# Kernel optimization log

Hardware: AMD Instinct MI355X
Metric: run time of the kernel (lower is better)

## Reference

```python
import jax, jax.numpy as jnp
import numpy as np

C_FINE, C_MID, C_COARSE = 100, 20, 5
EPS = 1e-12


def setup_inputs() -> dict:
    key = jax.random.key(0)
    k1, k2 = jax.random.split(key)
    N, D = 262144, 128
    representations = jax.random.normal(k1, (N, D), dtype=jnp.float32)
    target_fine = jax.random.randint(k2, (N,), 0, C_FINE, dtype=jnp.int32)
    # nested hierarchy: fine -> mid (5 fines per mid), fine -> coarse (20 fines per coarse)
    fine2mid = (jnp.arange(C_FINE, dtype=jnp.int32) // (C_FINE // C_MID)).astype(jnp.int32)
    fine2coarse = (jnp.arange(C_FINE, dtype=jnp.int32) // (C_FINE // C_COARSE)).astype(jnp.int32)
    return {
        "representations": representations,
        "target_fine": target_fine,
        "fine2mid": fine2mid,
        "fine2coarse": fine2coarse,
    }


def _safe_norm(diff):
    # L2 norm along last axis; eps gives a 0 subgradient at diff==0
    return jnp.sqrt(jnp.sum(diff * diff, axis=-1) + EPS)


def _segment_mean(x, ids, num_segments):
    ones = jnp.ones(x.shape[:1], x.dtype)
    s = jax.ops.segment_sum(x, ids, num_segments=num_segments)
    c = jax.ops.segment_sum(ones, ids, num_segments=num_segments)
    return s / jnp.maximum(c, 1.0)[:, None]


def reference(representations, target_fine, fine2mid, fine2coarse):
    # ---- tree construction (vectorized version of the per-class Python loops) ----
    # fine prototypes: mean of representations per fine class  [C_FINE, D]
    fine_protos = _segment_mean(representations, target_fine, C_FINE)
    # mid prototypes: mean of child fine prototypes  [C_MID, D]
    mid_protos = _segment_mean(fine_protos, fine2mid, C_MID)
    # coarse prototypes: mean of child mid prototypes  [C_COARSE, D]
    mid2coarse = jax.ops.segment_max(fine2coarse, fine2mid, num_segments=C_MID)
    coarse_protos = _segment_mean(mid_protos, mid2coarse, C_COARSE)
    # (the root node contributes ||root - root|| = 0 to every pair, so it is omitted)

    # ---- pairwise tree-path distances over all fine-class pairs ----
    iu, ju = np.triu_indices(C_FINE, k=1)  # static C*(C-1)/2 = 4950 pairs
    ci, cj = fine2coarse[iu], fine2coarse[ju]
    mi, mj = fine2mid[iu], fine2mid[ju]
    tree_d = _safe_norm(coarse_protos[ci] - coarse_protos[cj]) \
           + _safe_norm(mid_protos[mi] - mid_protos[mj])
    # Euclidean distances between fine prototypes
    proto_d = _safe_norm(fine_protos[iu] - fine_protos[ju])

    # ---- CPCC: loss = 1 - Pearson correlation(tree_d, proto_d) ----
    tc = tree_d - jnp.mean(tree_d)
    pc = proto_d - jnp.mean(proto_d)
    corr = jnp.sum(tc * pc) / jnp.sqrt(jnp.sum(tc * tc) * jnp.sum(pc * pc) + EPS)
    return 1.0 - corr
```

## Files before the change

kernel.cpp:

```cpp
#include <hip/hip_runtime.h>
#include <math.h>

#define C_FINE   100
#define C_MID    20
#define C_COARSE 5
#define D        128
#define NROWS    262144
#define NPAIRS   4950
#define NBLK4    78

#define NB       512
#define ROWS_PB  (NROWS/NB)
#define NSTEP    (ROWS_PB/32)
#define MT       7
#define PSTR2    (113*128)

#define FP_OFF    0
#define DM_OFF    12800
#define DC_OFF    13200
#define ACC_OFF   13232
#define DONE_OFF  13244
#define CNT_OFF   13248
#define FSUM_OFF  13376
#define PART_OFF  26176

typedef __attribute__((ext_vector_type(8))) short bf16x8;
typedef __attribute__((ext_vector_type(4))) float f32x4;

static __device__ __forceinline__ unsigned short f2bf(float f) {
    unsigned int x = __float_as_uint(f);
    x += 0x7FFF + ((x >> 16) & 1);
    return (unsigned short)(x >> 16);
}

__global__ __launch_bounds__(256) void kMF(const float* __restrict__ rep,
                                           const int* __restrict__ tgt,
                                           float* __restrict__ ws) {
    __shared__ int hist[128];
    const int t  = threadIdx.x;
    const int w  = t >> 6;
    const int l  = t & 63;
    const int lg = l >> 4;
    const int ll = l & 15;
    const int blk   = blockIdx.x;
    const int rbase = blk * ROWS_PB;

    if (t < 128) hist[t] = 0;
    __syncthreads();
    atomicAdd(&hist[tgt[rbase + t]], 1);
    atomicAdd(&hist[tgt[rbase + t + 256]], 1);

    const int colbase = 32 * w + ll;

    f32x4 acc[MT][2];
    #pragma unroll
    for (int m = 0; m < MT; ++m)
        #pragma unroll
        for (int n = 0; n < 2; ++n)
            #pragma unroll
            for (int i = 0; i < 4; ++i) acc[m][n][i] = 0.f;

    float vA[16], vB[16];
    int   tA[8],  tB[8];

#define LOADSTEP(V, T, s) do {                                                  \
    const float* p_ = rep + ((size_t)(rbase + (s) * 32 + 8 * lg) * D + colbase);\
    _Pragma("unroll")                                                           \
    for (int j_ = 0; j_ < 8; ++j_) {                                            \
        V[j_]     = p_[j_ * D];                                                 \
        V[8 + j_] = p_[j_ * D + 16];                                            \
    }                                                                           \
    const int* q_ = tgt + (rbase + (s) * 32 + 8 * lg);                          \
    _Pragma("unroll")                                                           \
    for (int j_ = 0; j_ < 8; ++j_) T[j_] = q_[j_];                              \
} while (0)

#define COMPSTEP(V, T) do {                                                     \
    bf16x8 b0_, b1_;                                                            \
    _Pragma("unroll")                                                           \
    for (int j_ = 0; j_ < 8; ++j_) {                                            \
        b0_[j_] = (short)f2bf(V[j_]);                                           \
        b1_[j_] = (short)f2bf(V[8 + j_]);                                       \
    }                                                                           \
    _Pragma("unroll")                                                           \
    for (int m_ = 0; m_ < MT; ++m_) {                                           \
        const int cb_ = 16 * m_ + ll;                                           \
        bf16x8 a_;                                                              \
        _Pragma("unroll")                                                       \
        for (int j_ = 0; j_ < 8; ++j_)                                          \
            a_[j_] = (T[j_] == cb_) ? (short)0x3F80 : (short)0;                 \
        acc[m_][0] = __builtin_amdgcn_mfma_f32_16x16x32_bf16(a_, b0_, acc[m_][0], 0, 0, 0); \
        acc[m_][1] = __builtin_amdgcn_mfma_f32_16x16x32_bf16(a_, b1_, acc[m_][1], 0, 0, 0); \
    }                                                                           \
} while (0)

    LOADSTEP(vA, tA, 0);
    #pragma unroll 1
    for (int s = 0; s < NSTEP; s += 2) {
        LOADSTEP(vB, tB, s + 1);
        COMPSTEP(vA, tA);
        if (s + 2 < NSTEP) LOADSTEP(vA, tA, s + 2);
        COMPSTEP(vB, tB);
    }
#undef LOADSTEP
#undef COMPSTEP

    float* part = ws + PART_OFF + (size_t)blk * PSTR2;
    #pragma unroll
    for (int m = 0; m < MT; ++m)
        #pragma unroll
        for (int n = 0; n < 2; ++n)
            #pragma unroll
            for (int i = 0; i < 4; ++i)
                part[(16 * m + 4 * lg + i) * D + 32 * w + 16 * n + ll] = acc[m][n][i];
    __syncthreads();
    if (t < 128) part[112 * D + t] = (t < C_FINE) ? (float)hist[t] : 0.f;
}

__global__ __launch_bounds__(512) void kRed(float* __restrict__ ws) {
    const int c = blockIdx.x;
    const int t = threadIdx.x;
    const int g = t >> 7, d = t & 127;
    float s = 0.f;
    #pragma unroll 8
    for (int b = g; b < NB; b += 4)
        s += ws[PART_OFF + (size_t)b * PSTR2 + c * D + d];
    __shared__ float red[4][128];
    red[g][d] = s;

    float cv = ws[PART_OFF + (size_t)t * PSTR2 + 112 * D + c];
    #pragma unroll
    for (int off = 32; off > 0; off >>= 1) cv += __shfl_down(cv, off);
    __shared__ float cw[8];
    if ((t & 63) == 0) cw[t >> 6] = cv;
    __syncthreads();
    if (g == 0) ws[FSUM_OFF + c * D + d] = red[0][d] + red[1][d] + red[2][d] + red[3][d];
    if (t == 0) {
        float tot = 0.f;
        #pragma unroll
        for (int q = 0; q < 8; ++q) tot += cw[q];
        ws[CNT_OFF + c] = tot;
    }
}

__global__ __launch_bounds__(256) void k3_hier(const int* __restrict__ f2m,
                                               const int* __restrict__ f2c,
                                               float* __restrict__ ws) {
    __shared__ float fineP[C_FINE][D];
    __shared__ float midP[C_MID][D + 1];
    __shared__ float coarP[C_COARSE][D + 1];
    __shared__ int   sf2m[C_FINE], sf2c[C_FINE], m2c[C_MID];
    __shared__ float midCnt[C_MID], coarCnt[C_COARSE];
    __shared__ float sTot[C_FINE];
    const int t = threadIdx.x;

    if (t < C_FINE) {
        sf2m[t] = f2m[t]; sf2c[t] = f2c[t];
        sTot[t] = ws[CNT_OFF + t];
    }
    for (int e = t; e < C_MID * (D + 1); e += 256) ((float*)midP)[e] = 0.f;
    for (int e = t; e < C_COARSE * (D + 1); e += 256) ((float*)coarP)[e] = 0.f;
    __syncthreads();

    for (int e = t; e < C_FINE * D; e += 256) {
        int c = e >> 7, d = e & 127;
        float v = ws[FSUM_OFF + e] / fmaxf(sTot[c], 1.f);
        fineP[c][d] = v;
        ws[FP_OFF + e] = v;
    }
    if (t < C_MID) {
        int cntv = 0, mx = -2147483647;
        for (int f = 0; f < C_FINE; ++f)
            if (sf2m[f] == t) { ++cntv; mx = max(mx, sf2c[f]); }
        midCnt[t] = (float)max(cntv, 1);
        m2c[t] = mx;
    }
    __syncthreads();

    if (t < D) {
        const int d = t;
        for (int f = 0; f < C_FINE; ++f)
            midP[sf2m[f]][d] += fineP[f][d];
        for (int m = 0; m < C_MID; ++m)
            midP[m][d] /= midCnt[m];
    }
    if (t >= 128 && t < 128 + C_COARSE) {
        int cc = t - 128, cntv = 0;
        for (int m = 0; m < C_MID; ++m) if (m2c[m] == cc) ++cntv;
        coarCnt[cc] = (float)max(cntv, 1);
    }
    __syncthreads();

    if (t < D) {
        const int d = t;
        for (int m = 0; m < C_MID; ++m)
            coarP[m2c[m]][d] += midP[m][d];
        for (int cc = 0; cc < C_COARSE; ++cc)
            coarP[cc][d] /= coarCnt[cc];
    }
    __syncthreads();

    for (int e = t; e < C_MID * C_MID; e += 256) {
        int m1 = e / C_MID, m2 = e % C_MID;
        float ss = 0.f;
        #pragma unroll 8
        for (int d = 0; d < D; ++d) {
            float df = midP[m1][d] - midP[m2][d];
            ss += df * df;
        }
        ws[DM_OFF + e] = sqrtf(ss + 1e-12f);
    }
    for (int e = t; e < C_COARSE * C_COARSE; e += 256) {
        int c1 = e / C_COARSE, c2 = e % C_COARSE;
        float ss = 0.f;
        #pragma unroll 8
        for (int d = 0; d < D; ++d) {
            float df = coarP[c1][d] - coarP[c2][d];
            ss += df * df;
        }
        ws[DC_OFF + e] = sqrtf(ss + 1e-12f);
    }
    if (t < 5) ((double*)(ws + ACC_OFF))[t] = 0.0;
    if (t == 5) ((int*)ws + DONE_OFF)[0] = 0;
}

__global__ __launch_bounds__(64) void k45_pairs(float* __restrict__ ws,
                                                const int* __restrict__ f2m,
                                                const int* __restrict__ f2c,
                                                float* __restrict__ out) {
    const int p = blockIdx.x * 64 + threadIdx.x;
    double st = 0, sp = 0, stp = 0, stt = 0, spp = 0;
    if (p < NPAIRS) {
        int i = 0, rem = p;
        while (rem >= C_FINE - 1 - i) { rem -= C_FINE - 1 - i; ++i; }
        int j = i + 1 + rem;

        const float4* Fi = (const float4*)(ws + FP_OFF + i * D);
        const float4* Fj = (const float4*)(ws + FP_OFF + j * D);
        float ss = 0.f;
        #pragma unroll
        for (int k = 0; k < D / 4; ++k) {
            float4 a = Fi[k], b = Fj[k];
            float dx = a.x - b.x, dy = a.y - b.y, dz = a.z - b.z, dw = a.w - b.w;
            ss += dx * dx + dy * dy + dz * dz + dw * dw;
        }
        float proto = sqrtf(ss + 1e-12f);
        float tree  = ws[DC_OFF + f2c[i] * C_COARSE + f2c[j]]
                    + ws[DM_OFF + f2m[i] * C_MID + f2m[j]];
        st = tree; sp = proto;
        stp = (double)tree * (double)proto;
        stt = (double)tree * (double)tree;
        spp = (double)proto * (double)proto;
    }
    for (int off = 32; off > 0; off >>= 1) {
        st  += __shfl_down(st, off);
        sp  += __shfl_down(sp, off);
        stp += __shfl_down(stp, off);
        stt += __shfl_down(stt, off);
        spp += __shfl_down(spp, off);
    }
    if (threadIdx.x == 0) {
        double* acc = (double*)(ws + ACC_OFF);
        atomicAdd(&acc[0], st);
        atomicAdd(&acc[1], sp);
        atomicAdd(&acc[2], stp);
        atomicAdd(&acc[3], stt);
        atomicAdd(&acc[4], spp);
        __threadfence();
        int* done = (int*)ws + DONE_OFF;
        int ticket = atomicAdd(done, 1);
        if (ticket == NBLK4 - 1) {
            double fst  = atomicAdd(&acc[0], 0.0);
            double fsp  = atomicAdd(&acc[1], 0.0);
            double fstp = atomicAdd(&acc[2], 0.0);
            double fstt = atomicAdd(&acc[3], 0.0);
            double fspp = atomicAdd(&acc[4], 0.0);
            const double n = (double)NPAIRS;
            double num = fstp - fst * fsp / n;
            double dtt = fstt - fst * fst / n;
            double dpp = fspp - fsp * fsp / n;
            double corr = num / sqrt(dtt * dpp + 1e-12);
            out[0] = (float)(1.0 - corr);
        }
    }
}

extern "C" void kernel_launch(void* const* d_in, const int* in_sizes, int n_in,
                              void* d_out, int out_size, void* d_ws, size_t ws_size,
                              hipStream_t stream) {
    const float* rep = (const float*)d_in[0];
    const int*   tgt = (const int*)d_in[1];
    const int*   f2m = (const int*)d_in[2];
    const int*   f2c = (const int*)d_in[3];
    float* ws  = (float*)d_ws;
    float* out = (float*)d_out;

    hipLaunchKernelGGL(kMF,       dim3(NB),     dim3(256), 0, stream, rep, tgt, ws);
    hipLaunchKernelGGL(kRed,      dim3(C_FINE), dim3(512), 0, stream, ws);
    hipLaunchKernelGGL(k3_hier,   dim3(1),      dim3(256), 0, stream, f2m, f2c, ws);
    hipLaunchKernelGGL(k45_pairs, dim3(NBLK4),  dim3(64),  0, stream,
                       ws, f2m, f2c, out);
}
```

Before: 81.99 us.

## Stage representation tiles through LDS with coalesced float4 loads in kMF

The segment-sum MFMA kernel now uses 512 threads per block, each wave owning 16 columns instead of 32. Each 32-row tile is loaded with coalesced float4 global reads into a double-buffered LDS tile, and targets are cached in LDS once. Previously each lane issued strided scalar global loads. The change aims to improve global memory coalescing and latency hiding. In exchange it adds LDS traffic and a __syncthreads per step.

Result: slower. 86.38 us (+5.4%).

```diff
diff --git a/kernel.cpp b/kernel.cpp
--- a/kernel.cpp
+++ b/kernel.cpp
@@ -33,10 +33,12 @@
     return (unsigned short)(x >> 16);
 }
 
-__global__ __launch_bounds__(256) void kMF(const float* __restrict__ rep,
-                                           const int* __restrict__ tgt,
-                                           float* __restrict__ ws) {
-    __shared__ int hist[128];
+__global__ __launch_bounds__(512, 4) void kMF(const float* __restrict__ rep,
+                                              const int* __restrict__ tgt,
+                                              float* __restrict__ ws) {
+    __shared__ float tile[2][32 * 128];
+    __shared__ int   ltgt[ROWS_PB];
+    __shared__ int   hist[128];
     const int t  = threadIdx.x;
     const int w  = t >> 6;
     const int l  = t & 63;
@@ -47,73 +49,72 @@
 
     if (t < 128) hist[t] = 0;
     __syncthreads();
-    atomicAdd(&hist[tgt[rbase + t]], 1);
-    atomicAdd(&hist[tgt[rbase + t + 256]], 1);
-
-    const int colbase = 32 * w + ll;
-
-    f32x4 acc[MT][2];
+    {
+        int c = tgt[rbase + t];
+        ltgt[t] = c;
+        atomicAdd(&hist[c], 1);
+    }
+
+    const float4* rep4 = (const float4*)rep;
+    const int tile4base = rbase * (D / 4);
+
+    f32x4 acc[MT];
     #pragma unroll
     for (int m = 0; m < MT; ++m)
         #pragma unroll
-        for (int n = 0; n < 2; ++n)
+        for (int i = 0; i < 4; ++i) acc[m][i] = 0.f;
+
+    {
+        float4 a0 = rep4[tile4base + t];
+        float4 a1 = rep4[tile4base + 512 + t];
+        ((float4*)tile[0])[t]       = a0;
+        ((float4*)tile[0])[t + 512] = a1;
+    }
+    __syncthreads();
+
+    #pragma unroll 1
+    for (int s = 0; s < NSTEP; ++s) {
+        const int buf = s & 1;
+        float4 na, nb;
+        if (s + 1 < NSTEP) {
+            na = rep4[tile4base + (s + 1) * 1024 + t];
+            nb = rep4[tile4base + (s + 1) * 1024 + 512 + t];
+        }
+
+        const float* tf = tile[buf];
+        float vB[8];
+        int   tv[8];
+        #pragma unroll
+        for (int j = 0; j < 8; ++j) {
+            vB[j] = tf[(8 * lg + j) * D + 16 * w + ll];
+            tv[j] = ltgt[s * 32 + 8 * lg + j];
+        }
+        bf16x8 b0;
+        #pragma unroll
+        for (int j = 0; j < 8; ++j) b0[j] = (short)f2bf(vB[j]);
+        #pragma unroll
+        for (int m = 0; m < MT; ++m) {
+            const int cb = 16 * m + ll;
+            bf16x8 a;
             #pragma unroll
-            for (int i = 0; i < 4; ++i) acc[m][n][i] = 0.f;
-
-    float vA[16], vB[16];
-    int   tA[8],  tB[8];
-
-#define LOADSTEP(V, T, s) do {                                                  \
-    const float* p_ = rep + ((size_t)(rbase + (s) * 32 + 8 * lg) * D + colbase);\
-    _Pragma("unroll")                                                           \
-    for (int j_ = 0; j_ < 8; ++j_) {                                            \
-        V[j_]     = p_[j_ * D];                                                 \
-        V[8 + j_] = p_[j_ * D + 16];                                            \
-    }                                                                           \
-    const int* q_ = tgt + (rbase + (s) * 32 + 8 * lg);                          \
-    _Pragma("unroll")                                                           \
-    for (int j_ = 0; j_ < 8; ++j_) T[j_] = q_[j_];                              \
-} while (0)
-
-#define COMPSTEP(V, T) do {                                                     \
-    bf16x8 b0_, b1_;                                                            \
-    _Pragma("unroll")                                                           \
-    for (int j_ = 0; j_ < 8; ++j_) {                                            \
-        b0_[j_] = (short)f2bf(V[j_]);                                           \
-        b1_[j_] = (short)f2bf(V[8 + j_]);                                       \
-    }                                                                           \
-    _Pragma("unroll")                                                           \
-    for (int m_ = 0; m_ < MT; ++m_) {                                           \
-        const int cb_ = 16 * m_ + ll;                                           \
-        bf16x8 a_;                                                              \
-        _Pragma("unroll")                                                       \
-        for (int j_ = 0; j_ < 8; ++j_)                                          \
-            a_[j_] = (T[j_] == cb_) ? (short)0x3F80 : (short)0;                 \
-        acc[m_][0] = __builtin_amdgcn_mfma_f32_16x16x32_bf16(a_, b0_, acc[m_][0], 0, 0, 0); \
-        acc[m_][1] = __builtin_amdgcn_mfma_f32_16x16x32_bf16(a_, b1_, acc[m_][1], 0, 0, 0); \
-    }                                                                           \
-} while (0)
-
-    LOADSTEP(vA, tA, 0);
-    #pragma unroll 1
-    for (int s = 0; s < NSTEP; s += 2) {
-        LOADSTEP(vB, tB, s + 1);
-        COMPSTEP(vA, tA);
-        if (s + 2 < NSTEP) LOADSTEP(vA, tA, s + 2);
-        COMPSTEP(vB, tB);
-    }
-#undef LOADSTEP
-#undef COMPSTEP
+            for (int j = 0; j < 8; ++j)
+                a[j] = (tv[j] == cb) ? (short)0x3F80 : (short)0;
+            acc[m] = __builtin_amdgcn_mfma_f32_16x16x32_bf16(a, b0, acc[m], 0, 0, 0);
+        }
+
+        if (s + 1 < NSTEP) {
+            ((float4*)tile[buf ^ 1])[t]       = na;
+            ((float4*)tile[buf ^ 1])[t + 512] = nb;
+        }
+        __syncthreads();
+    }
 
     float* part = ws + PART_OFF + (size_t)blk * PSTR2;
     #pragma unroll
     for (int m = 0; m < MT; ++m)
         #pragma unroll
-        for (int n = 0; n < 2; ++n)
-            #pragma unroll
-            for (int i = 0; i < 4; ++i)
-                part[(16 * m + 4 * lg + i) * D + 32 * w + 16 * n + ll] = acc[m][n][i];
-    __syncthreads();
+        for (int i = 0; i < 4; ++i)
+            part[(16 * m + 4 * lg + i) * D + 16 * w + ll] = acc[m][i];
     if (t < 128) part[112 * D + t] = (t < C_FINE) ? (float)hist[t] : 0.f;
 }
 
@@ -295,7 +296,7 @@
     float* ws  = (float*)d_ws;
     float* out = (float*)d_out;
 
-    hipLaunchKernelGGL(kMF,       dim3(NB),     dim3(256), 0, stream, rep, tgt, ws);
+    hipLaunchKernelGGL(kMF,       dim3(NB),     dim3(512), 0, stream, rep, tgt, ws);
     hipLaunchKernelGGL(kRed,      dim3(C_FINE), dim3(512), 0, stream, ws);
     hipLaunchKernelGGL(k3_hier,   dim3(1),      dim3(256), 0, stream, f2m, f2c, ws);
     hipLaunchKernelGGL(k45_pairs, dim3(NBLK4),  dim3(64),  0, stream,
```

## Use 1024-thread blocks with in-block LDS partial reduction and class-major partials

Applied to the files above, without the earlier changes.

The segment-sum kernel now runs 256 blocks of 1024 threads. Four row-groups of waves reduce their MFMA accumulators through shared-memory slabs before writing, which halves the number of partial-sum tiles sent to global memory. Target labels are staged once in LDS rather than reloaded per step. Partials and counts are laid out class-major, so the reduction kernel reads contiguously and only sums 256 partials. This adds serialized LDS accumulation passes with barriers, and may lower occupancy because of the larger block and LDS footprint.

Result: no change. 82.30 us (+0.4%).

```diff
diff --git a/kernel.cpp b/kernel.cpp
--- a/kernel.cpp
+++ b/kernel.cpp
@@ -9,11 +9,10 @@
 #define NPAIRS   4950
 #define NBLK4    78
 
-#define NB       512
-#define ROWS_PB  (NROWS/NB)
-#define NSTEP    (ROWS_PB/32)
+#define NB       256
+#define RPB      1024
+#define NSTEP    8
 #define MT       7
-#define PSTR2    (113*128)
 
 #define FP_OFF    0
 #define DM_OFF    12800
@@ -23,6 +22,7 @@
 #define CNT_OFF   13248
 #define FSUM_OFF  13376
 #define PART_OFF  26176
+#define CNTT_OFF  3696192
 
 typedef __attribute__((ext_vector_type(8))) short bf16x8;
 typedef __attribute__((ext_vector_type(4))) float f32x4;
@@ -33,24 +33,33 @@
     return (unsigned short)(x >> 16);
 }
 
-__global__ __launch_bounds__(256) void kMF(const float* __restrict__ rep,
-                                           const int* __restrict__ tgt,
-                                           float* __restrict__ ws) {
-    __shared__ int hist[128];
+__global__ __launch_bounds__(1024, 4) void kMF(const float* __restrict__ rep,
+                                               const int* __restrict__ tgt,
+                                               float* __restrict__ ws) {
+    __shared__ int   ltgt[RPB];
+    __shared__ int   hist[128];
+    __shared__ float slabs[4][112][33];
     const int t  = threadIdx.x;
-    const int w  = t >> 6;
+    const int wv = t >> 6;
+    const int rg = wv >> 2;
+    const int cw = wv & 3;
     const int l  = t & 63;
     const int lg = l >> 4;
     const int ll = l & 15;
     const int blk   = blockIdx.x;
-    const int rbase = blk * ROWS_PB;
+    const int rbase = blk * RPB;
 
     if (t < 128) hist[t] = 0;
     __syncthreads();
-    atomicAdd(&hist[tgt[rbase + t]], 1);
-    atomicAdd(&hist[tgt[rbase + t + 256]], 1);
-
-    const int colbase = 32 * w + ll;
+    {
+        int c = tgt[rbase + t];
+        ltgt[t] = c;
+        atomicAdd(&hist[c], 1);
+    }
+    __syncthreads();
+
+    const int rowbase = rg * 256;
+    const int colbase = 32 * cw + ll;
 
     f32x4 acc[MT][2];
     #pragma unroll
@@ -61,21 +70,22 @@
             for (int i = 0; i < 4; ++i) acc[m][n][i] = 0.f;
 
     float vA[16], vB[16];
-    int   tA[8],  tB[8];
-
-#define LOADSTEP(V, T, s) do {                                                  \
-    const float* p_ = rep + ((size_t)(rbase + (s) * 32 + 8 * lg) * D + colbase);\
+
+#define LOADSTEP(V, s) do {                                                     \
+    const float* p_ = rep + ((size_t)(rbase + rowbase + (s) * 32 + 8 * lg) * D  \
+                             + colbase);                                        \
     _Pragma("unroll")                                                           \
     for (int j_ = 0; j_ < 8; ++j_) {                                            \
         V[j_]     = p_[j_ * D];                                                 \
         V[8 + j_] = p_[j_ * D + 16];                                            \
     }                                                                           \
-    const int* q_ = tgt + (rbase + (s) * 32 + 8 * lg);                          \
+} while (0)
+
+#define COMPSTEP(V, s) do {                                                     \
+    int tv_[8];                                                                 \
     _Pragma("unroll")                                                           \
-    for (int j_ = 0; j_ < 8; ++j_) T[j_] = q_[j_];                              \
-} while (0)
-
-#define COMPSTEP(V, T) do {                                                     \
+    for (int j_ = 0; j_ < 8; ++j_)                                              \
+        tv_[j_] = ltgt[rowbase + (s) * 32 + 8 * lg + j_];                       \
     bf16x8 b0_, b1_;                                                            \
     _Pragma("unroll")                                                           \
     for (int j_ = 0; j_ < 8; ++j_) {                                            \
@@ -88,59 +98,67 @@
         bf16x8 a_;                                                              \
         _Pragma("unroll")                                                       \
         for (int j_ = 0; j_ < 8; ++j_)                                          \
-            a_[j_] = (T[j_] == cb_) ? (short)0x3F80 : (short)0;                 \
+            a_[j_] = (tv_[j_] == cb_) ? (short)0x3F80 : (short)0;               \
         acc[m_][0] = __builtin_amdgcn_mfma_f32_16x16x32_bf16(a_, b0_, acc[m_][0], 0, 0, 0); \
         acc[m_][1] = __builtin_amdgcn_mfma_f32_16x16x32_bf16(a_, b1_, acc[m_][1], 0, 0, 0); \
     }                                                                           \
 } while (0)
 
-    LOADSTEP(vA, tA, 0);
+    LOADSTEP(vA, 0);
     #pragma unroll 1
     for (int s = 0; s < NSTEP; s += 2) {
-        LOADSTEP(vB, tB, s + 1);
-        COMPSTEP(vA, tA);
-        if (s + 2 < NSTEP) LOADSTEP(vA, tA, s + 2);
-        COMPSTEP(vB, tB);
+        LOADSTEP(vB, s + 1);
+        COMPSTEP(vA, s);
+        if (s + 2 < NSTEP) LOADSTEP(vA, s + 2);
+        COMPSTEP(vB, s + 1);
     }
 #undef LOADSTEP
 #undef COMPSTEP
 
-    float* part = ws + PART_OFF + (size_t)blk * PSTR2;
-    #pragma unroll
-    for (int m = 0; m < MT; ++m)
-        #pragma unroll
-        for (int n = 0; n < 2; ++n)
+    #pragma unroll 1
+    for (int r = 0; r < 4; ++r) {
+        if (rg == r) {
             #pragma unroll
-            for (int i = 0; i < 4; ++i)
-                part[(16 * m + 4 * lg + i) * D + 32 * w + 16 * n + ll] = acc[m][n][i];
-    __syncthreads();
-    if (t < 128) part[112 * D + t] = (t < C_FINE) ? (float)hist[t] : 0.f;
-}
-
-__global__ __launch_bounds__(512) void kRed(float* __restrict__ ws) {
+            for (int m = 0; m < MT; ++m)
+                #pragma unroll
+                for (int n = 0; n < 2; ++n)
+                    #pragma unroll
+                    for (int i = 0; i < 4; ++i) {
+                        const int cls = 16 * m + 4 * lg + i;
+                        const int col = 16 * n + ll;
+                        if (r == 0) slabs[cw][cls][col] = acc[m][n][i];
+                        else        slabs[cw][cls][col] += acc[m][n][i];
+                    }
+        }
+        __syncthreads();
+    }
+
+    for (int e = t; e < 112 * 128; e += 1024) {
+        const int c = e >> 7, d = e & 127;
+        ws[PART_OFF + ((size_t)c * NB + blk) * 128 + d] = slabs[d >> 5][c][d & 31];
+    }
+    if (t < 128) ws[CNTT_OFF + t * NB + blk] = (float)hist[t];
+}
+
+__global__ __launch_bounds__(256) void kRed(float* __restrict__ ws) {
     const int c = blockIdx.x;
     const int t = threadIdx.x;
     const int g = t >> 7, d = t & 127;
+    const float* base = ws + PART_OFF + (size_t)c * NB * 128;
     float s = 0.f;
     #pragma unroll 8
-    for (int b = g; b < NB; b += 4)
-        s += ws[PART_OFF + (size_t)b * PSTR2 + c * D + d];
-    __shared__ float red[4][128];
+    for (int b = g; b < NB; b += 2) s += base[b * 128 + d];
+    __shared__ float red[2][128];
     red[g][d] = s;
 
-    float cv = ws[PART_OFF + (size_t)t * PSTR2 + 112 * D + c];
+    float cv = ws[CNTT_OFF + c * NB + t];
     #pragma unroll
     for (int off = 32; off > 0; off >>= 1) cv += __shfl_down(cv, off);
-    __shared__ float cw[8];
+    __shared__ float cw[4];
     if ((t & 63) == 0) cw[t >> 6] = cv;
     __syncthreads();
-    if (g == 0) ws[FSUM_OFF + c * D + d] = red[0][d] + red[1][d] + red[2][d] + red[3][d];
-    if (t == 0) {
-        float tot = 0.f;
-        #pragma unroll
-        for (int q = 0; q < 8; ++q) tot += cw[q];
-        ws[CNT_OFF + c] = tot;
-    }
+    if (g == 0) ws[FSUM_OFF + c * D + d] = red[0][d] + red[1][d];
+    if (t == 0) ws[CNT_OFF + c] = cw[0] + cw[1] + cw[2] + cw[3];
 }
 
 __global__ __launch_bounds__(256) void k3_hier(const int* __restrict__ f2m,
@@ -295,9 +313,9 @@
     float* ws  = (float*)d_ws;
     float* out = (float*)d_out;
 
-    hipLaunchKernelGGL(kMF,       dim3(NB),     dim3(256), 0, stream, rep, tgt, ws);
-    hipLaunchKernelGGL(kRed,      dim3(C_FINE), dim3(512), 0, stream, ws);
-    hipLaunchKernelGGL(k3_hier,   dim3(1),      dim3(256), 0, stream, f2m, f2c, ws);
-    hipLaunchKernelGGL(k45_pairs, dim3(NBLK4),  dim3(64),  0, stream,
+    hipLaunchKernelGGL(kMF,       dim3(NB),     dim3(1024), 0, stream, rep, tgt, ws);
+    hipLaunchKernelGGL(kRed,      dim3(C_FINE), dim3(256),  0, stream, ws);
+    hipLaunchKernelGGL(k3_hier,   dim3(1),      dim3(256),  0, stream, f2m, f2c, ws);
+    hipLaunchKernelGGL(k45_pairs, dim3(NBLK4),  dim3(64),   0, stream,
                        ws, f2m, f2c, out);
 }
```
